# Kernel tuning notes

Hardware: AMD Instinct MI355X
Metric: run time of the kernel (lower is better)

## Reference

```python
import jax, jax.numpy as jnp
import numpy as np

N_NODES = 100000
N_EDGES = 1000000
N_GRAPHS = 512
IN_DIM = 3
HID = 64


def setup_inputs() -> dict:
    key = jax.random.key(0)
    ks = jax.random.split(key, 7)
    x = jax.random.normal(ks[0], (N_NODES, IN_DIM), dtype=jnp.float32)
    edge_index = jax.random.randint(ks[1], (2, N_EDGES), 0, N_NODES, dtype=jnp.int64)
    batch = jnp.sort(jax.random.randint(ks[2], (N_NODES,), 0, N_GRAPHS, dtype=jnp.int64))
    # Glorot-ish init for GCNConv linear weights (PyG uses glorot), zero bias.
    W1 = jax.random.normal(ks[3], (IN_DIM, HID), dtype=jnp.float32) / np.float32(np.sqrt(IN_DIM))
    b1 = jnp.zeros((HID,), dtype=jnp.float32)
    W2 = jax.random.normal(ks[4], (HID, HID), dtype=jnp.float32) / np.float32(np.sqrt(HID))
    b2 = jnp.zeros((HID,), dtype=jnp.float32)
    return {"x": x, "W1": W1, "b1": b1, "W2": W2, "b2": b2,
            "edge_index": edge_index, "batch": batch}


def reference(x, W1, b1, W2, b2, edge_index, batch):
    n = x.shape[0]
    loop = jnp.arange(n)
    # GCNConv adds self-loops, then symmetric normalization D^-1/2 (A+I) D^-1/2
    src = jnp.concatenate([edge_index[0], loop])  # [E+N]
    dst = jnp.concatenate([edge_index[1], loop])  # [E+N]
    deg = jax.ops.segment_sum(jnp.ones(dst.shape[0], x.dtype), dst, num_segments=n)
    dinv = jnp.where(deg > 0, jax.lax.rsqrt(deg), 0.0)
    norm = dinv[src] * dinv[dst]  # [E+N]

    def gcn_conv(h, W, b):
        hw = h @ W                       # [N, out] linear first (PyG order)
        msg = hw[src] * norm[:, None]    # gather + scale, [E+N, out]
        agg = jax.ops.segment_sum(msg, dst, num_segments=n)  # scatter-add
        return agg + b

    h = jax.nn.relu(gcn_conv(x, W1, b1))
    h = jax.nn.relu(gcn_conv(h, W2, b2))

    # global_mean_pool over the batch vector
    sums = jax.ops.segment_sum(h, batch, num_segments=N_GRAPHS)          # [G, HID]
    counts = jax.ops.segment_sum(jnp.ones(n, h.dtype), batch, num_segments=N_GRAPHS)
    return sums / jnp.maximum(counts, 1.0)[:, None]
```

## Files before the change

### kernel.cpp

```cpp
#include <hip/hip_runtime.h>

#define HID 64
#define N_GRAPHS_C 512
#define BSHIFT 8
#define NBUCK_MAX 512
#define CAP 3264
#define EPB 4096

typedef unsigned short u16;
typedef unsigned int u32;
typedef unsigned long long u64;

__device__ __forceinline__ float bf2f(u16 u) {
    union { u32 i; float f; } v; v.i = ((u32)u) << 16; return v.f;
}
__device__ __forceinline__ u16 f2bf(float f) {
    union { float f; u32 i; } v; v.f = f;
    u32 x = v.i;
    return (u16)((x + 0x7fffu + ((x >> 16) & 1u)) >> 16);
}


__device__ __forceinline__ int lower_bound(const int* __restrict__ a, int n, int key) {
    int lo = 0, hi = n;
    while (lo < hi) {
        int mid = (lo + hi) >> 1;
        if (a[mid] < key) lo = mid + 1; else hi = mid;
    }
    return lo;
}

__global__ void prep(int* __restrict__ gcursor, const int* __restrict__ batch,
                     int* __restrict__ gstart, int n, int nGraphs) {
    int t = threadIdx.x;
    gcursor[t] = 0;
    for (int g = t; g <= nGraphs; g += 512)
        gstart[g] = lower_bound(batch, n, g);
}


__global__ void bin_pairs(const int* __restrict__ src, const int* __restrict__ dst,
                          int* __restrict__ gcursor, u32* __restrict__ pairs,
                          int nE, int nbuck) {
    __shared__ int lh[NBUCK_MAX];
    __shared__ int lbase[NBUCK_MAX];
    int t = threadIdx.x;
    lh[t] = 0;
    __syncthreads();
    int base = blockIdx.x * EPB;
    u32 pk[8]; int rj[8], bj[8];
    #pragma unroll
    for (int j = 0; j < 8; ++j) {
        int e = base + j * 512 + t;
        if (e < nE) {
            int s = src[e], d = dst[e];
            bj[j] = d >> BSHIFT;
            pk[j] = ((u32)(d & 255) << 17) | (u32)s;
            rj[j] = atomicAdd(&lh[bj[j]], 1);
        } else {
            bj[j] = -1;
        }
    }
    __syncthreads();
    if (t < nbuck) lbase[t] = (lh[t] > 0) ? atomicAdd(&gcursor[t], lh[t]) : 0;
    __syncthreads();
    #pragma unroll
    for (int j = 0; j < 8; ++j) {
        if (bj[j] >= 0) {
            int pos = bj[j] * CAP + lbase[bj[j]] + rj[j];
            pairs[pos] = pk[j];
        }
    }
}

__global__ void build_csr(const u32* __restrict__ pairs, const int* __restrict__ gcursor,
                          int* __restrict__ csr_src, int2* __restrict__ off2,
                          float* __restrict__ dinv, const float* __restrict__ x,
                          float4* __restrict__ xs, u16* __restrict__ A16, int n) {
    __shared__ int hist[256];
    __shared__ int tmp[256];
    int t = threadIdx.x;
    int b = blockIdx.x;
    int pbeg = b * CAP;
    int pend = pbeg + gcursor[b];
    if (t < 256) hist[t] = 0;
    if (b == 0 && t < 32) ((u32*)(A16 + (size_t)n * HID))[t] = 0;
    __syncthreads();
    for (int i = pbeg + t; i < pend; i += 512)
        atomicAdd(&hist[pairs[i] >> 17], 1);
    __syncthreads();
    int v = 0;
    if (t < 256) { v = hist[t]; tmp[t] = v; }
    __syncthreads();
    for (int d = 1; d < 256; d <<= 1) {
        int add = (t >= d && t < 256) ? tmp[t - d] : 0;
        __syncthreads();
        if (t < 256) tmp[t] += add;
        __syncthreads();
    }
    if (t < 256) {
        int e = pbeg + tmp[t] - v;
        int node = (b << BSHIFT) + t;
        if (node < n) {
            float dv = rsqrtf((float)(v + 1));
            off2[node] = make_int2(e, e + v);
            dinv[node] = dv;
            xs[node] = make_float4(x[3*node]*dv, x[3*node+1]*dv, x[3*node+2]*dv, dv);
        }
        hist[t] = e;
    }
    __syncthreads();
    for (int i = pbeg + t; i < pend; i += 512) {
        u32 p = pairs[i];
        int pos = atomicAdd(&hist[p >> 17], 1);
        csr_src[pos] = (int)(p & 0x1FFFFu);
    }
}


__global__ void agg3(const float4* __restrict__ xs, const int* __restrict__ csr_src,
                     const int2* __restrict__ off2, float4* __restrict__ agg4, int n) {
    int node = blockIdx.x * blockDim.x + threadIdx.x;
    if (node >= n) return;
    int2 be = off2[node];
    int beg = be.x, end = be.y;
    float4 self = xs[node];
    float a0 = 0.f, a1 = 0.f, a2 = 0.f;
    for (int k = beg; k < end; k += 8) {
        int e1 = end - 1;
        int idx[8];
        float4 v[8];
        #pragma unroll
        for (int j = 0; j < 8; ++j) idx[j] = csr_src[min(k + j, e1)];
        #pragma unroll
        for (int j = 0; j < 8; ++j) v[j] = xs[idx[j]];
        #pragma unroll
        for (int j = 0; j < 8; ++j) {
            if (k + j < end) { a0 += v[j].x; a1 += v[j].y; a2 += v[j].z; }
        }
    }
    agg4[node] = make_float4(a0 + self.x, a1 + self.y, a2 + self.z, self.w);
}


#define MM2_NODES 32
__global__ void mm2f(const float4* __restrict__ agg4, const float* __restrict__ W1,
                     const float* __restrict__ b1, const float* __restrict__ W2,
                     u16* __restrict__ A16, int n) {
    __shared__ float w[HID * HID];
    __shared__ float h[MM2_NODES * HID];
    __shared__ float dd[MM2_NODES];
    int t = threadIdx.x;
    for (int i = t; i < HID * HID; i += 256) w[i] = W2[i];
    int base = blockIdx.x * MM2_NODES;
    for (int i = t; i < MM2_NODES * HID; i += 256) {
        int node = base + (i >> 6);
        int f = i & 63;
        float hv = 0.0f;
        if (node < n) {
            float4 a = agg4[node];
            float v = (a.x * W1[f] + a.y * W1[HID + f] + a.z * W1[2 * HID + f]) * a.w + b1[f];
            hv = v > 0.0f ? v : 0.0f;
            if (f == 0) dd[i >> 6] = a.w;
        }
        h[i] = hv;
    }
    __syncthreads();
    int f = t & 63, g = t >> 6;
    float acc[8];
    #pragma unroll
    for (int j = 0; j < 8; ++j) acc[j] = 0.0f;
    #pragma unroll 4
    for (int k = 0; k < HID; ++k) {
        float wk = w[k * HID + f];
        #pragma unroll
        for (int j = 0; j < 8; ++j) acc[j] += h[(g * 8 + j) * HID + k] * wk;
    }
    #pragma unroll
    for (int j = 0; j < 8; ++j) {
        int node = base + g * 8 + j;
        if (node < n) A16[(size_t)node * HID + f] = f2bf(acc[j] * dd[g * 8 + j]);
    }
}


__global__ void gather_nodes(const u16* __restrict__ A16, const float* __restrict__ dinv,
                             const int* __restrict__ csr_src, const int2* __restrict__ off2,
                             const float* __restrict__ bias,
                             u16* __restrict__ H16, int n) {
    int t = threadIdx.x;
    int waveq = t >> 4;
    int m = t & 15;
    int qbase = t & 48;
    int node = blockIdx.x * 16 + waveq;
    if (node >= n) return;
    int2 be = off2[node];
    int beg = be.x, end = be.y;
    u64 selfrow = *(const u64*)(A16 + ((size_t)node << 6) + (m << 2));
    u32 slo = (u32)selfrow, shi = (u32)(selfrow >> 32);
    float acc0 = bf2f((u16)(slo & 0xffffu));
    float acc1 = bf2f((u16)(slo >> 16));
    float acc2 = bf2f((u16)(shi & 0xffffu));
    float acc3 = bf2f((u16)(shi >> 16));
    const char* Ab = (const char*)A16;
    u32 laneoff = (u32)(m << 3);
    for (int k = beg; k < end; k += 8) {
        int lim = min(end - k, 8);
        int myIdx = (m < lim) ? csr_src[k + m] : n;
        int ss[8]; u64 rows[8];
        #pragma unroll
        for (int j = 0; j < 8; ++j)
            ss[j] = __shfl(myIdx, qbase + j, 64);
        #pragma unroll
        for (int j = 0; j < 8; ++j)
            rows[j] = *(const u64*)(Ab + (((u32)ss[j] << 7) | laneoff));
        #pragma unroll
        for (int j = 0; j < 8; ++j) {
            u32 lo = (u32)rows[j], hi = (u32)(rows[j] >> 32);
            acc0 += bf2f((u16)(lo & 0xffffu));
            acc1 += bf2f((u16)(lo >> 16));
            acc2 += bf2f((u16)(hi & 0xffffu));
            acc3 += bf2f((u16)(hi >> 16));
        }
    }
    float ddv = dinv[node];
    float4 bb = *(const float4*)(bias + (m << 2));
    float v0 = fmaxf(acc0 * ddv + bb.x, 0.0f);
    float v1 = fmaxf(acc1 * ddv + bb.y, 0.0f);
    float v2 = fmaxf(acc2 * ddv + bb.z, 0.0f);
    float v3 = fmaxf(acc3 * ddv + bb.w, 0.0f);
    u64 outp = (u64)f2bf(v0) | ((u64)f2bf(v1) << 16)
             | ((u64)f2bf(v2) << 32) | ((u64)f2bf(v3) << 48);
    *(u64*)(H16 + ((size_t)node << 6) + (m << 2)) = outp;
}


__global__ void pool_graph(const u16* __restrict__ H16, const int* __restrict__ gstart,
                           float* __restrict__ out, int n) {
    int g = blockIdx.x;
    int t = threadIdx.x;
    int lo = gstart[g];
    int hi = gstart[g + 1];
    int cntN = hi - lo;
    int sid = t >> 4;
    int m = t & 15;
    float a0 = 0.f, a1 = 0.f, a2 = 0.f, a3 = 0.f;
    int i = lo + sid;
    for (; i + 16 < hi; i += 32) {
        u64 r0 = *(const u64*)(H16 + ((size_t)i << 6) + (m << 2));
        u64 r1 = *(const u64*)(H16 + ((size_t)(i + 16) << 6) + (m << 2));
        u32 l0 = (u32)r0, h0 = (u32)(r0 >> 32);
        u32 l1 = (u32)r1, h1 = (u32)(r1 >> 32);
        a0 += bf2f((u16)(l0 & 0xffffu)) + bf2f((u16)(l1 & 0xffffu));
        a1 += bf2f((u16)(l0 >> 16))     + bf2f((u16)(l1 >> 16));
        a2 += bf2f((u16)(h0 & 0xffffu)) + bf2f((u16)(h1 & 0xffffu));
        a3 += bf2f((u16)(h0 >> 16))     + bf2f((u16)(h1 >> 16));
    }
    if (i < hi) {
        u64 r0 = *(const u64*)(H16 + ((size_t)i << 6) + (m << 2));
        u32 l0 = (u32)r0, h0 = (u32)(r0 >> 32);
        a0 += bf2f((u16)(l0 & 0xffffu));
        a1 += bf2f((u16)(l0 >> 16));
        a2 += bf2f((u16)(h0 & 0xffffu));
        a3 += bf2f((u16)(h0 >> 16));
    }
    a0 += __shfl_xor(a0, 16, 64); a0 += __shfl_xor(a0, 32, 64);
    a1 += __shfl_xor(a1, 16, 64); a1 += __shfl_xor(a1, 32, 64);
    a2 += __shfl_xor(a2, 16, 64); a2 += __shfl_xor(a2, 32, 64);
    a3 += __shfl_xor(a3, 16, 64); a3 += __shfl_xor(a3, 32, 64);
    __shared__ float smf[4 * HID];
    int wave = t >> 6, lane = t & 63;
    if (lane < 16) {
        smf[wave * HID + 4 * lane + 0] = a0;
        smf[wave * HID + 4 * lane + 1] = a1;
        smf[wave * HID + 4 * lane + 2] = a2;
        smf[wave * HID + 4 * lane + 3] = a3;
    }
    __syncthreads();
    if (t < HID) {
        float s = smf[t] + smf[HID + t] + smf[2 * HID + t] + smf[3 * HID + t];
        out[(size_t)g * HID + t] = s / fmaxf((float)cntN, 1.0f);
    }
}


extern "C" void kernel_launch(void* const* d_in, const int* in_sizes, int n_in,
                              void* d_out, int out_size, void* d_ws, size_t ws_size,
                              hipStream_t stream) {
    const float* x  = (const float*)d_in[0];
    const float* W1 = (const float*)d_in[1];
    const float* b1 = (const float*)d_in[2];
    const float* W2 = (const float*)d_in[3];
    const float* b2 = (const float*)d_in[4];
    const int*   ei = (const int*)d_in[5];
    const int*   batch = (const int*)d_in[6];

    const int n  = in_sizes[0] / 3;
    const int nE = in_sizes[5] / 2;
    const int* src = ei;
    const int* dst = ei + nE;
    const int nbuck = (n + ((1 << BSHIFT) - 1)) >> BSHIFT;
    const int nGraphs = out_size / HID;

    char* p = (char*)d_ws;
    int*    gcursor = (int*)p;                p += 2048;
    int*    gstart  = (int*)p;                p += 4096;
    int*    csr_src = (int*)p;                p += (size_t)nbuck * CAP * 4;
    int2*   off2    = (int2*)p;               p += (size_t)n * 8;
    float*  dinv    = (float*)p;              p += (size_t)n * 4;
    float4* xs      = (float4*)p;             p += (size_t)n * 16;
    float4* agg4    = (float4*)p;             p += (size_t)n * 16;
    u16*    A16     = (u16*)p;                p += (size_t)(n + 1) * HID * 2;
    u16*    H2      = (u16*)p;                p += (size_t)n * HID * 2;
    u32*    pairs   = (u32*)A16;

    const int BT = 256;
    const int gridNode = (n + BT - 1) / BT;
    const int gridE2   = (nE + EPB - 1) / EPB;
    const int gridMM2  = (n + MM2_NODES - 1) / MM2_NODES;
    const int gridGath = (n + 15) / 16;

    prep<<<1, 512, 0, stream>>>(gcursor, batch, gstart, n, nGraphs);
    bin_pairs<<<gridE2, 512, 0, stream>>>(src, dst, gcursor, pairs, nE, nbuck);
    build_csr<<<nbuck, 512, 0, stream>>>(pairs, gcursor, csr_src, off2, dinv, x, xs, A16, n);

    agg3<<<gridNode, BT, 0, stream>>>(xs, csr_src, off2, agg4, n);
    mm2f<<<gridMM2, BT, 0, stream>>>(agg4, W1, b1, W2, A16, n);

    gather_nodes<<<gridGath, BT, 0, stream>>>(A16, dinv, csr_src, off2, b2, H2, n);

    pool_graph<<<nGraphs, BT, 0, stream>>>(H2, gstart, (float*)d_out, n);
}
```

Before: 169.1 us.

## Register-tile the dense layer-2 matmul with transposed hidden tile and packed stores

Rewrites the per-node 64x64 matmul kernel to handle 128 nodes per block. The hidden activations are stored transposed in shared memory and each thread computes an 8-node by 4-feature register tile using float4 shared loads. W1 and b1 are staged in shared memory, and bf16 outputs are packed into 64-bit stores. The goal is fewer shared-memory loads per FMA, fewer W2 reloads per node, and wider global writes, in exchange for more registers and shared memory per block.

Result: faster. 160.4 us (-5.1%).

```diff
diff --git a/kernel.cpp b/kernel.cpp
--- a/kernel.cpp
+++ b/kernel.cpp
@@ -143,43 +143,80 @@
 }
 
 
-#define MM2_NODES 32
-__global__ void mm2f(const float4* __restrict__ agg4, const float* __restrict__ W1,
+#define MMN 128
+__global__ void mm2r(const float4* __restrict__ agg4, const float* __restrict__ W1,
                      const float* __restrict__ b1, const float* __restrict__ W2,
                      u16* __restrict__ A16, int n) {
     __shared__ float w[HID * HID];
-    __shared__ float h[MM2_NODES * HID];
-    __shared__ float dd[MM2_NODES];
-    int t = threadIdx.x;
+    __shared__ float hT[HID][MMN];
+    __shared__ float dd[MMN];
+    __shared__ float w1s[4 * HID];
+    int t = threadIdx.x;
+
     for (int i = t; i < HID * HID; i += 256) w[i] = W2[i];
-    int base = blockIdx.x * MM2_NODES;
-    for (int i = t; i < MM2_NODES * HID; i += 256) {
-        int node = base + (i >> 6);
-        int f = i & 63;
-        float hv = 0.0f;
-        if (node < n) {
-            float4 a = agg4[node];
-            float v = (a.x * W1[f] + a.y * W1[HID + f] + a.z * W1[2 * HID + f]) * a.w + b1[f];
-            hv = v > 0.0f ? v : 0.0f;
-            if (f == 0) dd[i >> 6] = a.w;
-        }
-        h[i] = hv;
-    }
-    __syncthreads();
-    int f = t & 63, g = t >> 6;
-    float acc[8];
-    #pragma unroll
-    for (int j = 0; j < 8; ++j) acc[j] = 0.0f;
+    if (t < HID) {
+        w1s[t]           = W1[t];
+        w1s[HID + t]     = W1[HID + t];
+        w1s[2 * HID + t] = W1[2 * HID + t];
+        w1s[3 * HID + t] = b1[t];
+    }
+    int base = blockIdx.x * MMN;
+    int nl = t & 127;
+    int node1 = base + nl;
+    float4 a = make_float4(0.f, 0.f, 0.f, 0.f);
+    bool valid = (node1 < n);
+    if (valid) a = agg4[node1];
+    if (t < MMN) dd[t] = a.w;
+    __syncthreads();
+
+    int fbase = t >> 7;
+    #pragma unroll
+    for (int s = 0; s < 32; ++s) {
+        int f = fbase + 2 * s;
+        float v = 0.f;
+        if (valid) {
+            v = (a.x * w1s[f] + a.y * w1s[HID + f] + a.z * w1s[2 * HID + f]) * a.w
+                + w1s[3 * HID + f];
+            v = v > 0.f ? v : 0.f;
+        }
+        hT[f][nl] = v;
+    }
+    __syncthreads();
+
+    int fq = t & 15, oct = t >> 4;
+    int nb = oct * 8;
+    float acc[8][4];
+    #pragma unroll
+    for (int j = 0; j < 8; ++j)
+        #pragma unroll
+        for (int q = 0; q < 4; ++q) acc[j][q] = 0.f;
+
     #pragma unroll 4
     for (int k = 0; k < HID; ++k) {
-        float wk = w[k * HID + f];
-        #pragma unroll
-        for (int j = 0; j < 8; ++j) acc[j] += h[(g * 8 + j) * HID + k] * wk;
-    }
+        float4 w4 = *(const float4*)&w[k * HID + fq * 4];
+        float4 h0 = *(const float4*)&hT[k][nb];
+        float4 h1 = *(const float4*)&hT[k][nb + 4];
+        float hv[8] = { h0.x, h0.y, h0.z, h0.w, h1.x, h1.y, h1.z, h1.w };
+        #pragma unroll
+        for (int j = 0; j < 8; ++j) {
+            acc[j][0] += hv[j] * w4.x;
+            acc[j][1] += hv[j] * w4.y;
+            acc[j][2] += hv[j] * w4.z;
+            acc[j][3] += hv[j] * w4.w;
+        }
+    }
+
     #pragma unroll
     for (int j = 0; j < 8; ++j) {
-        int node = base + g * 8 + j;
-        if (node < n) A16[(size_t)node * HID + f] = f2bf(acc[j] * dd[g * 8 + j]);
+        int node = base + nb + j;
+        if (node < n) {
+            float dj = dd[nb + j];
+            u64 outp = (u64)f2bf(acc[j][0] * dj)
+                     | ((u64)f2bf(acc[j][1] * dj) << 16)
+                     | ((u64)f2bf(acc[j][2] * dj) << 32)
+                     | ((u64)f2bf(acc[j][3] * dj) << 48);
+            *(u64*)(A16 + ((size_t)node << 6) + (fq << 2)) = outp;
+        }
     }
 }
 
@@ -317,7 +354,7 @@
     const int BT = 256;
     const int gridNode = (n + BT - 1) / BT;
     const int gridE2   = (nE + EPB - 1) / EPB;
-    const int gridMM2  = (n + MM2_NODES - 1) / MM2_NODES;
+    const int gridMM2  = (n + MMN - 1) / MMN;
     const int gridGath = (n + 15) / 16;
 
     prep<<<1, 512, 0, stream>>>(gcursor, batch, gstart, n, nGraphs);
@@ -325,7 +362,7 @@
     build_csr<<<nbuck, 512, 0, stream>>>(pairs, gcursor, csr_src, off2, dinv, x, xs, A16, n);
 
     agg3<<<gridNode, BT, 0, stream>>>(xs, csr_src, off2, agg4, n);
-    mm2f<<<gridMM2, BT, 0, stream>>>(agg4, W1, b1, W2, A16, n);
+    mm2r<<<gridMM2, BT, 0, stream>>>(agg4, W1, b1, W2, A16, n);
 
     gather_nodes<<<gridGath, BT, 0, stream>>>(A16, dinv, csr_src, off2, b2, H2, n);
 
```
